# Kernel optimization log

Hardware: AMD Instinct MI355X
Metric: run time of the kernel (lower is better)

## Reference

```python
import jax, jax.numpy as jnp
import numpy as np

N = 512       # num_nodes (feature dim of x == num_nodes, per GCNConv(num_nodes, f1))
BZ = 32       # subjects
TC = 256      # tc_length
F1 = 256
F2 = 128
E = 524288    # edges in the given (corr) graph over all bz*N nodes
NTOT = BZ * N
SLOPE = 0.2   # leaky relu negative_slope


def setup_inputs() -> dict:
    key = jax.random.key(0)
    ks = jax.random.split(key, 17)
    w = lambda k, shape: (jax.random.normal(k, shape, jnp.float32) * (shape[-1] ** -0.5))
    return {
        "x": jax.random.normal(ks[0], (NTOT, N), jnp.float32),
        "t": jax.random.normal(ks[1], (NTOT, TC), jnp.float32),
        "gumbel_u": jax.random.uniform(ks[2], (BZ, N, N, 2), jnp.float32),
        "edge_index": jax.random.randint(ks[3], (2, E), 0, NTOT, jnp.int64 if jax.config.jax_enable_x64 else jnp.int32),
        "conv1_w": w(ks[4], (F1, N)),
        "conv1_b": jnp.zeros((F1,), jnp.float32),
        "conv2_w": w(ks[5], (F2, F1)),
        "conv2_b": jnp.zeros((F2,), jnp.float32),
        "fc_cat_w": w(ks[6], (2, 2 * TC)),
        "fc_cat_b": jnp.zeros((2,), jnp.float32),
        "fcn1_w": w(ks[7], (256, F2 * 2 * N)),
        "fcn1_b": jnp.zeros((256,), jnp.float32),
        "fcn2_w": w(ks[8], (32, 256)),
        "fcn2_b": jnp.zeros((32,), jnp.float32),
        "fcn3_w": w(ks[9], (2, 32)),
        "fcn3_b": jnp.zeros((2,), jnp.float32),
    }


def _gcn_dense(x, A, W, b):
    # PyG GCNConv on a dense 0/1 adjacency A (edge r->c means A[r,c]=1):
    # add self loop, in-degree symmetric norm, aggregate sources into targets.
    n = A.shape[0]
    Ah = A + jnp.eye(n, dtype=A.dtype)
    deg = Ah.sum(axis=0)                                  # in-degree (targets = cols)
    dis = jnp.where(deg > 0, jax.lax.rsqrt(deg), 0.0)
    M = dis[:, None] * Ah * dis[None, :]                  # M[j,i] = d_j^-1/2 A_hat[j,i] d_i^-1/2
    return M.T @ (x @ W.T) + b


def _gcn_sparse(x, row, col, W, b):
    n = x.shape[0]
    loops = jnp.arange(n, dtype=row.dtype)
    r = jnp.concatenate([row, loops])
    c = jnp.concatenate([col, loops])
    deg = jax.ops.segment_sum(jnp.ones_like(c, x.dtype), c, num_segments=n)
    dis = jnp.where(deg > 0, jax.lax.rsqrt(deg), 0.0)
    norm = dis[r] * dis[c]                                # [E+n]
    xw = x @ W.T                                          # [n, out]
    out = jax.ops.segment_sum(xw[r] * norm[:, None], c, num_segments=n)
    return out + b


def reference(x, t, gumbel_u, edge_index, conv1_w, conv1_b, conv2_w, conv2_b,
              fc_cat_w, fc_cat_b, fcn1_w, fcn1_b, fcn2_w, fcn2_b, fcn3_w, fcn3_b):
    bz = t.shape[0] // N
    tb = t.reshape(bz, N, -1)
    xb = x.reshape(bz, N, -1)
    # fc_cat(relu(cat([senders, receivers]))) factors into per-node terms:
    Ws = fc_cat_w[:, :TC]   # multiplies senders half
    Wr = fc_cat_w[:, TC:]   # multiplies receivers half

    def per_sample(ti, xi, ui):
        u = jax.nn.relu(ti)                               # [N, TC]
        ls = u @ Ws.T                                     # [N, 2] sender term
        lr = u @ Wr.T                                     # [N, 2] receiver term
        # pair k = i*N+j has receiver t_i, sender t_j
        logits = lr[:, None, :] + ls[None, :, :] + fc_cat_b   # [N, N, 2]
        g = -jnp.log(-jnp.log(jnp.clip(ui, 1e-9, 1.0 - 1e-9)))  # Gumbel(0,1)
        y = logits + g                                    # tau = 1
        A = (jnp.argmax(y, axis=-1) == 0).astype(xi.dtype)    # hard sample, class 0 => edge
        A = jax.lax.stop_gradient(A)                      # torch.where -> indices blocks grad
        h = jax.nn.relu(_gcn_dense(xi, A, conv1_w, conv1_b))
        return _gcn_dense(h, A, conv2_w, conv2_b)         # [N, F2]

    x_op = jax.vmap(per_sample)(tb, xb, gumbel_u)         # [bz, N, F2]

    row, col = edge_index[0], edge_index[1]
    x_corr = jax.nn.relu(_gcn_sparse(x, row, col, conv1_w, conv1_b))
    x_corr = _gcn_sparse(x_corr, row, col, conv2_w, conv2_b)   # [bz*N, F2]

    emb = jnp.concatenate([x_op.reshape(-1, F2), x_corr], axis=1)  # [bz*N, 2*F2]
    emb = emb.reshape(bz, -1)                             # [bz, 2*F2*N]
    h = jax.nn.leaky_relu(emb @ fcn1_w.T + fcn1_b, SLOPE)
    h = jax.nn.leaky_relu(h @ fcn2_w.T + fcn2_b, SLOPE)
    return h @ fcn3_w.T + fcn3_b                          # [bz, 2]
```

## Files before the change

kernel.cpp:

```cpp
#include <hip/hip_runtime.h>
#include <hip/hip_bf16.h>

typedef __bf16 bf16_t;
typedef __bf16 bf16x8 __attribute__((ext_vector_type(8)));
typedef __bf16 bf16x4 __attribute__((ext_vector_type(4)));
typedef float f32x4 __attribute__((ext_vector_type(4)));

constexpr int kN = 512;
constexpr int kBZ = 32;
constexpr int kTC = 256;
constexpr int kE = 524288;
constexpr int kNTOT = 16384;

__global__ __launch_bounds__(256) void k_cvt3(const float* __restrict__ c1w, const float* __restrict__ c2w,
                                              bf16_t* __restrict__ c1b, bf16_t* __restrict__ c2b,
                                              int* __restrict__ counts, float* __restrict__ degsum) {
    int i = blockIdx.x * 256 + threadIdx.x;
    const int n0 = 32768, n1 = n0 + 8192, n2 = n1 + 4096, n3 = n2 + 4096;
    if (i < n0) {
        float4 v = ((const float4*)c1w)[i];
        bf16x4 o = {(bf16_t)v.x, (bf16_t)v.y, (bf16_t)v.z, (bf16_t)v.w};
        ((bf16x4*)c1b)[i] = o;
    } else if (i < n1) {
        int j = i - n0;
        float4 v = ((const float4*)c2w)[j];
        bf16x4 o = {(bf16_t)v.x, (bf16_t)v.y, (bf16_t)v.z, (bf16_t)v.w};
        ((bf16x4*)c2b)[j] = o;
    } else if (i < n2) {
        ((int4*)counts)[i - n1] = make_int4(0, 0, 0, 0);
    } else if (i < n3) {
        ((float4*)degsum)[i - n2] = make_float4(0.f, 0.f, 0.f, 0.f);
    }
}

__global__ __launch_bounds__(256) void k_lsr(const float* __restrict__ tin, const float* __restrict__ fcw,
                                             const float* __restrict__ fcb, float4* __restrict__ lsr) {
    int row = blockIdx.x * 4 + (threadIdx.x >> 6);
    int lane = threadIdx.x & 63;
    const float* tr = tin + (size_t)row * kTC;
    float s0 = 0, s1 = 0, r0 = 0, r1 = 0;
    for (int k = lane; k < kTC; k += 64) {
        float u = fmaxf(tr[k], 0.f);
        s0 += u * fcw[k];
        s1 += u * fcw[512 + k];
        r0 += u * fcw[256 + k];
        r1 += u * fcw[768 + k];
    }
#pragma unroll
    for (int off = 32; off > 0; off >>= 1) {
        s0 += __shfl_down(s0, off); s1 += __shfl_down(s1, off);
        r0 += __shfl_down(r0, off); r1 += __shfl_down(r1, off);
    }
    if (lane == 0) lsr[row] = make_float4(s0 + fcb[0], s1 + fcb[1], r0, r1);
}

__global__ __launch_bounds__(256) void k_adj(const float* __restrict__ gum, const float4* __restrict__ lsr,
                                             bf16_t* __restrict__ AT, float* __restrict__ degsum) {
    int s = blockIdx.z;
    int a0 = blockIdx.y * 64, b0 = blockIdx.x * 64;
    __shared__ bf16_t tile[64][72];
    int t = threadIdx.x;
    int lb = t & 63, ra = t >> 6;
    int b = b0 + lb;
    float4 pb = lsr[s * kN + b];
#pragma unroll 4
    for (int p = 0; p < 16; p++) {
        int a = a0 + p * 4 + ra;
        float4 qa = lsr[s * kN + a];
        const float* g = gum + ((((size_t)s * kN + a) * kN + b) << 1);
        float u0 = fmaxf(g[0], 1e-9f);
        float u1 = fmaxf(g[1], 1e-9f);
        float g0 = -__logf(-__logf(u0));
        float g1 = -__logf(-__logf(u1));
        float v = ((qa.z + pb.x + g0) >= (qa.w + pb.y + g1)) ? 1.f : 0.f;
        if (a == b) v += 1.f;
        tile[lb][p * 4 + ra] = (bf16_t)v;
    }
    __syncthreads();
    int rj = t >> 3, li = (t & 7) * 8;
#pragma unroll
    for (int p = 0; p < 2; p++) {
        int j = p * 32 + rj;
        bf16x8 v = *(const bf16x8*)&tile[j][li];
        *(bf16x8*)(AT + ((size_t)s * kN + b0 + j) * kN + a0 + li) = v;
        float ps = 0;
#pragma unroll
        for (int q = 0; q < 8; q++) ps += (float)v[q];
        ps += __shfl_down(ps, 4);
        ps += __shfl_down(ps, 2);
        ps += __shfl_down(ps, 1);
        if ((t & 7) == 0) atomicAdd(degsum + s * kN + b0 + j, ps);
    }
}

template <int MODE>
__global__ __launch_bounds__(256) void k_gemm(const bf16_t* __restrict__ A, const bf16_t* __restrict__ B,
                                              bf16_t* __restrict__ C, int K, int lda, int ldb, int ldc,
                                              size_t sA, size_t sB, size_t sC,
                                              const float* __restrict__ degsum, const float* __restrict__ bias) {
    int m0 = blockIdx.x * 128, n0 = blockIdx.y * 128, s = blockIdx.z;
    A += sA * s; B += sB * s; C += sC * s;
    __shared__ bf16_t As[128][72], Bs[128][72];
    f32x4 acc[4][4] = {};
    int tid = threadIdx.x;
    int wave = tid >> 6, lane = tid & 63;
    int wm = (wave & 1) * 64, wn = (wave >> 1) * 64;
    int fm = lane & 15, fq = lane >> 4;
    int srow = tid >> 3, scol = (tid & 7) * 8;
    for (int kb = 0; kb < K; kb += 64) {
        __syncthreads();
#pragma unroll
        for (int p = 0; p < 4; p++) {
            int row = p * 32 + srow;
            *(uint4*)&As[row][scol] = *(const uint4*)(A + (size_t)(m0 + row) * lda + kb + scol);
            *(uint4*)&Bs[row][scol] = *(const uint4*)(B + (size_t)(n0 + row) * ldb + kb + scol);
        }
        __syncthreads();
#pragma unroll
        for (int kk = 0; kk < 2; kk++) {
            bf16x8 af[4], bfr[4];
#pragma unroll
            for (int i = 0; i < 4; i++) {
                af[i] = *(const bf16x8*)&As[wm + i * 16 + fm][kk * 32 + fq * 8];
                bfr[i] = *(const bf16x8*)&Bs[wn + i * 16 + fm][kk * 32 + fq * 8];
            }
#pragma unroll
            for (int i = 0; i < 4; i++)
#pragma unroll
                for (int j = 0; j < 4; j++)
                    acc[i][j] = __builtin_amdgcn_mfma_f32_16x16x32_bf16(af[i], bfr[j], acc[i][j], 0, 0, 0);
        }
    }
#pragma unroll
    for (int i = 0; i < 4; i++) {
#pragma unroll
        for (int r = 0; r < 4; r++) {
            int row = wm + i * 16 + fq * 4 + r;
            float sc = rsqrtf(degsum[(size_t)s * kN + m0 + row]);
#pragma unroll
            for (int j = 0; j < 4; j++) {
                int col = n0 + wn + j * 16 + fm;
                float v = sc * acc[i][j][r] + bias[col];
                if constexpr (MODE == 1) v = fmaxf(v, 0.f);
                C[(size_t)(m0 + row) * ldc + col] = (bf16_t)v;
            }
        }
    }
}

template <bool AF32, int F, int DENSE_ROWS>
__global__ __launch_bounds__(256) void k_gemmT(const void* __restrict__ Ap, const bf16_t* __restrict__ B,
                                               bf16_t* __restrict__ XW, bf16_t* __restrict__ ZT, int K,
                                               const float* __restrict__ degsum) {
    int m0 = blockIdx.x * 128, n0 = blockIdx.y * 128;
    __shared__ __align__(16) bf16_t smem[2 * 128 * 72];
    bf16_t* AsBase = smem;
    bf16_t* BsBase = smem + 128 * 72;
    f32x4 acc[4][4] = {};
    int tid = threadIdx.x;
    int wave = tid >> 6, lane = tid & 63;
    int wm = (wave & 1) * 64, wn = (wave >> 1) * 64;
    int fm = lane & 15, fq = lane >> 4;
    int srow = tid >> 3, scol = (tid & 7) * 8;
    for (int kb = 0; kb < K; kb += 64) {
        __syncthreads();
#pragma unroll
        for (int p = 0; p < 4; p++) {
            int row = p * 32 + srow;
            if constexpr (AF32) {
                const float* ap = (const float*)Ap + (size_t)(m0 + row) * K + kb + scol;
                float4 lo = *(const float4*)ap;
                float4 hi = *(const float4*)(ap + 4);
                bf16x8 o = {(bf16_t)lo.x, (bf16_t)lo.y, (bf16_t)lo.z, (bf16_t)lo.w,
                            (bf16_t)hi.x, (bf16_t)hi.y, (bf16_t)hi.z, (bf16_t)hi.w};
                *(bf16x8*)&AsBase[row * 72 + scol] = o;
            } else {
                *(uint4*)&AsBase[row * 72 + scol] =
                    *(const uint4*)((const bf16_t*)Ap + (size_t)(m0 + row) * K + kb + scol);
            }
            *(uint4*)&BsBase[row * 72 + scol] = *(const uint4*)(B + (size_t)(n0 + row) * K + kb + scol);
        }
        __syncthreads();
#pragma unroll
        for (int kk = 0; kk < 2; kk++) {
            bf16x8 af[4], bfr[4];
#pragma unroll
            for (int i = 0; i < 4; i++) {
                af[i] = *(const bf16x8*)&AsBase[(wm + i * 16 + fm) * 72 + kk * 32 + fq * 8];
                bfr[i] = *(const bf16x8*)&BsBase[(wn + i * 16 + fm) * 72 + kk * 32 + fq * 8];
            }
#pragma unroll
            for (int i = 0; i < 4; i++)
#pragma unroll
                for (int j = 0; j < 4; j++)
                    acc[i][j] = __builtin_amdgcn_mfma_f32_16x16x32_bf16(af[i], bfr[j], acc[i][j], 0, 0, 0);
        }
    }
    bool doT = (m0 < DENSE_ROWS);
    __syncthreads();
#pragma unroll
    for (int i = 0; i < 4; i++) {
#pragma unroll
        for (int r = 0; r < 4; r++) {
            int row = wm + i * 16 + fq * 4 + r;
            float sc = doT ? rsqrtf(degsum[m0 + row]) : 0.f;
#pragma unroll
            for (int j = 0; j < 4; j++) {
                int col = wn + j * 16 + fm;
                float v = acc[i][j][r];
                XW[(size_t)(m0 + row) * F + n0 + col] = (bf16_t)v;
                if (doT) smem[col * 136 + row] = (bf16_t)(sc * v);
            }
        }
    }
    if (doT) {
        __syncthreads();
        int fr = tid >> 1, hi = (tid & 1) * 64;
        bf16_t* zrow = ZT + ((size_t)(m0 >> 9) * F + n0 + fr) * kN + (m0 & 511) + hi;
#pragma unroll
        for (int q = 0; q < 8; q++)
            *(bf16x8*)(zrow + q * 8) = *(const bf16x8*)&smem[fr * 136 + hi + q * 8];
    }
}


__global__ __launch_bounds__(256) void k_hist(const int* __restrict__ col, int* __restrict__ counts) {
    int e = blockIdx.x * 256 + threadIdx.x;
    if (e < kE) atomicAdd(&counts[col[e]], 1);
}

__global__ __launch_bounds__(256) void k_scan(const int* __restrict__ counts, int* __restrict__ offsets,
                                              int* __restrict__ cursor, float* __restrict__ dis_s) {
    __shared__ int ldc_[16896];
    __shared__ int sums[256];
    int t = threadIdx.x;
#define IDX(j) ((j) + ((j) >> 5))
    for (int i = 0; i < 64; i++) {
        int g = i * 256 + t;
        int c = counts[g];
        ldc_[IDX(g)] = c;
        dis_s[g] = rsqrtf((float)(c + 1));
    }
    __syncthreads();
    int s = 0;
    for (int i = 0; i < 64; i++) s += ldc_[IDX(t * 64 + i)];
    sums[t] = s;
    __syncthreads();
    for (int off = 1; off < 256; off <<= 1) {
        int y = (t >= off) ? sums[t - off] : 0;
        __syncthreads();
        sums[t] += y;
        __syncthreads();
    }
    int run = sums[t] - s;
    for (int i = 0; i < 64; i++) {
        int j = t * 64 + i;
        int c = ldc_[IDX(j)];
        ldc_[IDX(j)] = run;
        run += c;
    }
    __syncthreads();
    for (int i = 0; i < 64; i++) {
        int g = i * 256 + t;
        int o = ldc_[IDX(g)];
        offsets[g] = o;
        cursor[g] = o;
    }
#undef IDX
}

__global__ __launch_bounds__(256) void k_fill(const int* __restrict__ row, const int* __restrict__ col,
                                              int* __restrict__ cursor, int* __restrict__ list) {
    int e = blockIdx.x * 256 + threadIdx.x;
    if (e < kE) {
        int p = atomicAdd(&cursor[col[e]], 1);
        list[p] = row[e];
    }
}

template <int F, bool RELU>
__global__ __launch_bounds__(256) void k_sagg(const bf16_t* __restrict__ XW, int rowOffIn,
                                              const int* __restrict__ list, const int* __restrict__ offsets,
                                              const int* __restrict__ counts, const float* __restrict__ dis_s,
                                              const float* __restrict__ bias, bf16_t* __restrict__ OUT,
                                              int outColOff) {
    constexpr int TPR = F / 8;
    constexpr int RPB = 256 / TPR;
    int j = blockIdx.x * RPB + threadIdx.x / TPR;
    int f8 = (threadIdx.x % TPR) * 8;
    float dj = dis_s[j];
    const bf16_t* base = XW + (size_t)rowOffIn * F;
    float acc[8];
    {
        bf16x8 v = *(const bf16x8*)(base + (size_t)j * F + f8);
#pragma unroll
        for (int q = 0; q < 8; q++) acc[q] = dj * (float)v[q];
    }
    int off = offsets[j], cnt = counts[j];
    int e = 0;
    for (; e + 4 <= cnt; e += 4) {
        int r0 = list[off + e], r1 = list[off + e + 1], r2 = list[off + e + 2], r3 = list[off + e + 3];
        float d0 = dis_s[r0], d1 = dis_s[r1], d2 = dis_s[r2], d3 = dis_s[r3];
        bf16x8 v0 = *(const bf16x8*)(base + (size_t)r0 * F + f8);
        bf16x8 v1 = *(const bf16x8*)(base + (size_t)r1 * F + f8);
        bf16x8 v2 = *(const bf16x8*)(base + (size_t)r2 * F + f8);
        bf16x8 v3 = *(const bf16x8*)(base + (size_t)r3 * F + f8);
#pragma unroll
        for (int q = 0; q < 8; q++)
            acc[q] += (d0 * (float)v0[q] + d1 * (float)v1[q]) + (d2 * (float)v2[q] + d3 * (float)v3[q]);
    }
    for (; e < cnt; e++) {
        int r = list[off + e];
        float d = dis_s[r];
        bf16x8 v = *(const bf16x8*)(base + (size_t)r * F + f8);
#pragma unroll
        for (int q = 0; q < 8; q++) acc[q] += d * (float)v[q];
    }
    bf16x8 o;
#pragma unroll
    for (int q = 0; q < 8; q++) {
        float v = dj * acc[q] + bias[f8 + q];
        if (RELU) v = fmaxf(v, 0.f);
        o[q] = (bf16_t)v;
    }
    *(bf16x8*)(OUT + (size_t)j * 256 + outColOff + f8) = o;
}

__global__ __launch_bounds__(256) void k_fcn1(const bf16_t* __restrict__ EMB, const float* __restrict__ W1,
                                              float* __restrict__ partials) {
    int tid = threadIdx.x, wave = tid >> 6, lane = tid & 63;
    int fm = lane & 15, fq = lane >> 4;
    int kb0 = blockIdx.x * 128;
    f32x4 acc[2][4] = {};
#pragma unroll
    for (int ks = 0; ks < 128; ks += 32) {
        int k = kb0 + ks + fq * 8;
        bf16x8 a0 = *(const bf16x8*)(EMB + (size_t)fm * 131072 + k);
        bf16x8 a1 = *(const bf16x8*)(EMB + (size_t)(16 + fm) * 131072 + k);
        bf16x8 bfr[4];
#pragma unroll
        for (int j = 0; j < 4; j++) {
            int n = wave * 64 + j * 16 + fm;
            const float* p = W1 + (size_t)n * 131072 + k;
            float4 lo = *(const float4*)p;
            float4 hi = *(const float4*)(p + 4);
            bf16x8 b = {(bf16_t)lo.x, (bf16_t)lo.y, (bf16_t)lo.z, (bf16_t)lo.w,
                        (bf16_t)hi.x, (bf16_t)hi.y, (bf16_t)hi.z, (bf16_t)hi.w};
            bfr[j] = b;
        }
#pragma unroll
        for (int j = 0; j < 4; j++) {
            acc[0][j] = __builtin_amdgcn_mfma_f32_16x16x32_bf16(a0, bfr[j], acc[0][j], 0, 0, 0);
            acc[1][j] = __builtin_amdgcn_mfma_f32_16x16x32_bf16(a1, bfr[j], acc[1][j], 0, 0, 0);
        }
    }
    float* P = partials + (size_t)blockIdx.x * 8192;
#pragma unroll
    for (int i = 0; i < 2; i++)
#pragma unroll
        for (int j = 0; j < 4; j++)
#pragma unroll
            for (int r = 0; r < 4; r++)
                P[(size_t)(i * 16 + fq * 4 + r) * 256 + wave * 64 + j * 16 + fm] = acc[i][j][r];
}

__global__ __launch_bounds__(256) void k_reduce(const float* __restrict__ partials, float* __restrict__ part2) {
    int kg = blockIdx.x >> 5, eb = blockIdx.x & 31;
    int e = eb * 256 + threadIdx.x;
    float s = 0;
#pragma unroll 8
    for (int i = 0; i < 128; i++) s += partials[(size_t)(kg * 128 + i) * 8192 + e];
    part2[(size_t)kg * 8192 + e] = s;
}

__global__ __launch_bounds__(256) void k_head(const float* __restrict__ part2, const float* __restrict__ b1,
                                              const float* __restrict__ W2, const float* __restrict__ b2,
                                              const float* __restrict__ W3, const float* __restrict__ b3,
                                              float* __restrict__ out) {
    __shared__ float h1s[32][256];
    __shared__ float h2s[32][32];
    int t = threadIdx.x;
    for (int i = 0; i < 32; i++) {
        int e = i * 256 + t;
        float s = 0;
#pragma unroll
        for (int kg = 0; kg < 8; kg++) s += part2[kg * 8192 + e];
        s += b1[t];
        h1s[i][t] = (s > 0.f) ? s : 0.2f * s;
    }
    __syncthreads();
    for (int p = 0; p < 4; p++) {
        int id = p * 256 + t, si = id >> 5, o2 = id & 31;
        float s = 0;
        for (int k = 0; k < 256; k++) s += h1s[si][k] * W2[o2 * 256 + k];
        s += b2[o2];
        h2s[si][o2] = (s > 0.f) ? s : 0.2f * s;
    }
    __syncthreads();
    if (t < 64) {
        int si = t >> 1, o3 = t & 1;
        float s = 0;
#pragma unroll
        for (int k = 0; k < 32; k++) s += h2s[si][k] * W3[o3 * 32 + k];
        out[si * 2 + o3] = s + b3[o3];
    }
}


extern "C" void kernel_launch(void* const* d_in, const int* in_sizes, int n_in,
                              void* d_out, int out_size, void* d_ws, size_t ws_size,
                              hipStream_t stream) {
    const float* x = (const float*)d_in[0];
    const float* t = (const float*)d_in[1];
    const float* gum = (const float*)d_in[2];
    const int* eidx = (const int*)d_in[3];
    const float* c1w = (const float*)d_in[4];
    const float* c1b = (const float*)d_in[5];
    const float* c2w = (const float*)d_in[6];
    const float* c2b = (const float*)d_in[7];
    const float* fcw = (const float*)d_in[8];
    const float* fcb = (const float*)d_in[9];
    const float* w1 = (const float*)d_in[10];
    const float* b1 = (const float*)d_in[11];
    const float* w2 = (const float*)d_in[12];
    const float* b2 = (const float*)d_in[13];
    const float* w3 = (const float*)d_in[14];
    const float* b3 = (const float*)d_in[15];
    float* out = (float*)d_out;
    (void)in_sizes; (void)n_in; (void)out_size; (void)ws_size;

    char* ws = (char*)d_ws;
    size_t off = 0;
    auto alloc = [&](size_t bytes) -> char* {
        char* p = ws + off;
        off += (bytes + 255) & ~size_t(255);
        return p;
    };
    bf16_t* c1wb = (bf16_t*)alloc((size_t)256 * 512 * 2);
    bf16_t* c2wb = (bf16_t*)alloc((size_t)128 * 256 * 2);
    float4* lsr = (float4*)alloc((size_t)kNTOT * 16);
    bf16_t* AT = (bf16_t*)alloc((size_t)kBZ * kN * kN * 2);
    float* degsum = (float*)alloc((size_t)kNTOT * 4);
    bf16_t* XW1_EMB = (bf16_t*)alloc((size_t)kNTOT * 256 * 2);
    bf16_t* Z1T = (bf16_t*)alloc((size_t)kBZ * 256 * 512 * 2);
    bf16_t* H = (bf16_t*)alloc((size_t)32768 * 256 * 2);
    bf16_t* XW2 = (bf16_t*)alloc((size_t)32768 * 128 * 2);
    bf16_t* Z2T = (bf16_t*)alloc((size_t)kBZ * 128 * 512 * 2);
    int* counts = (int*)alloc((size_t)kNTOT * 4);
    int* offsets = (int*)alloc((size_t)kNTOT * 4);
    int* cursor = (int*)alloc((size_t)kNTOT * 4);
    float* diss = (float*)alloc((size_t)kNTOT * 4);
    int* list = (int*)alloc((size_t)kE * 4);
    float* partials = (float*)alloc((size_t)1024 * 8192 * 4);
    float* part2 = (float*)alloc((size_t)8 * 8192 * 4);

    bf16_t* XW1 = XW1_EMB;
    bf16_t* EMB = XW1_EMB;

    k_cvt3<<<192, 256, 0, stream>>>(c1w, c2w, c1wb, c2wb, counts, degsum);
    k_lsr<<<4096, 256, 0, stream>>>(t, fcw, fcb, lsr);
    k_adj<<<dim3(8, 8, 32), 256, 0, stream>>>(gum, lsr, AT, degsum);
    k_hist<<<2048, 256, 0, stream>>>(eidx + kE, counts);
    k_scan<<<1, 256, 0, stream>>>(counts, offsets, cursor, diss);
    k_fill<<<2048, 256, 0, stream>>>(eidx, eidx + kE, cursor, list);
    k_gemmT<true, 256, kNTOT><<<dim3(128, 2, 1), 256, 0, stream>>>(x, c1wb, XW1, Z1T, 512, degsum);
    k_gemm<1><<<dim3(4, 2, 32), 256, 0, stream>>>(AT, Z1T, H, 512, 512, 512, 256,
                                                  (size_t)512 * 512, (size_t)256 * 512, (size_t)512 * 256,
                                                  degsum, c1b);
    k_sagg<256, true><<<2048, 256, 0, stream>>>(XW1, 0, list, offsets, counts, diss, c1b,
                                                H + (size_t)16384 * 256, 0);
    k_gemmT<false, 128, kNTOT><<<dim3(256, 1, 1), 256, 0, stream>>>(H, c2wb, XW2, Z2T, 256, degsum);
    k_gemm<2><<<dim3(4, 1, 32), 256, 0, stream>>>(AT, Z2T, EMB, 512, 512, 512, 256,
                                                  (size_t)512 * 512, (size_t)128 * 512, (size_t)512 * 256,
                                                  degsum, c2b);
    k_sagg<128, false><<<1024, 256, 0, stream>>>(XW2, 16384, list, offsets, counts, diss, c2b, EMB, 128);
    k_fcn1<<<1024, 256, 0, stream>>>(EMB, w1, partials);
    k_reduce<<<256, 256, 0, stream>>>(partials, part2);
    k_head<<<1, 256, 0, stream>>>(part2, b1, w2, b2, w3, b3, out);
}
```

Before: 517.3 us.

## Merge dense and sparse GCN aggregation launches and pre-convert fcn1 weights in spare blocks

Merges the prep kernels (lsr and weight conversion) into a single launch. Each GCN layer's batched dense adjacency GEMM and its sparse edge-gather aggregation now run as block ranges of one kernel, so the two independent paths share a launch and fill the GPU together. The layer-1 launch also carries extra blocks that convert the large fcn1 weight (fp32) to bf16 into a new buffer, and fcn1 then reads bf16 instead of converting on the fly. This halves fcn1's weight traffic. In exchange it adds a full fp32 read and bf16 write of that weight, plus mixes heterogeneous block types in one kernel.

```diff
diff --git a/kernel.cpp b/kernel.cpp
--- a/kernel.cpp
+++ b/kernel.cpp
@@ -12,46 +12,48 @@
 constexpr int kE = 524288;
 constexpr int kNTOT = 16384;
 
-__global__ __launch_bounds__(256) void k_cvt3(const float* __restrict__ c1w, const float* __restrict__ c2w,
-                                              bf16_t* __restrict__ c1b, bf16_t* __restrict__ c2b,
+__global__ __launch_bounds__(256) void k_prep(const float* __restrict__ tin, const float* __restrict__ fcw,
+                                              const float* __restrict__ fcb, float4* __restrict__ lsr,
+                                              const float* __restrict__ c1w, const float* __restrict__ c2w,
+                                              bf16_t* __restrict__ c1wb, bf16_t* __restrict__ c2wb,
                                               int* __restrict__ counts, float* __restrict__ degsum) {
-    int i = blockIdx.x * 256 + threadIdx.x;
-    const int n0 = 32768, n1 = n0 + 8192, n2 = n1 + 4096, n3 = n2 + 4096;
-    if (i < n0) {
-        float4 v = ((const float4*)c1w)[i];
-        bf16x4 o = {(bf16_t)v.x, (bf16_t)v.y, (bf16_t)v.z, (bf16_t)v.w};
-        ((bf16x4*)c1b)[i] = o;
-    } else if (i < n1) {
-        int j = i - n0;
-        float4 v = ((const float4*)c2w)[j];
-        bf16x4 o = {(bf16_t)v.x, (bf16_t)v.y, (bf16_t)v.z, (bf16_t)v.w};
-        ((bf16x4*)c2b)[j] = o;
-    } else if (i < n2) {
-        ((int4*)counts)[i - n1] = make_int4(0, 0, 0, 0);
-    } else if (i < n3) {
-        ((float4*)degsum)[i - n2] = make_float4(0.f, 0.f, 0.f, 0.f);
-    }
-}
-
-__global__ __launch_bounds__(256) void k_lsr(const float* __restrict__ tin, const float* __restrict__ fcw,
-                                             const float* __restrict__ fcb, float4* __restrict__ lsr) {
-    int row = blockIdx.x * 4 + (threadIdx.x >> 6);
-    int lane = threadIdx.x & 63;
-    const float* tr = tin + (size_t)row * kTC;
-    float s0 = 0, s1 = 0, r0 = 0, r1 = 0;
-    for (int k = lane; k < kTC; k += 64) {
-        float u = fmaxf(tr[k], 0.f);
-        s0 += u * fcw[k];
-        s1 += u * fcw[512 + k];
-        r0 += u * fcw[256 + k];
-        r1 += u * fcw[768 + k];
-    }
-#pragma unroll
-    for (int off = 32; off > 0; off >>= 1) {
-        s0 += __shfl_down(s0, off); s1 += __shfl_down(s1, off);
-        r0 += __shfl_down(r0, off); r1 += __shfl_down(r1, off);
-    }
-    if (lane == 0) lsr[row] = make_float4(s0 + fcb[0], s1 + fcb[1], r0, r1);
+    int b = blockIdx.x;
+    if (b < 4096) {
+        int row = b * 4 + (threadIdx.x >> 6);
+        int lane = threadIdx.x & 63;
+        const float* tr = tin + (size_t)row * kTC;
+        float s0 = 0, s1 = 0, r0 = 0, r1 = 0;
+        for (int k = lane; k < kTC; k += 64) {
+            float u = fmaxf(tr[k], 0.f);
+            s0 += u * fcw[k];
+            s1 += u * fcw[512 + k];
+            r0 += u * fcw[256 + k];
+            r1 += u * fcw[768 + k];
+        }
+#pragma unroll
+        for (int off = 32; off > 0; off >>= 1) {
+            s0 += __shfl_down(s0, off); s1 += __shfl_down(s1, off);
+            r0 += __shfl_down(r0, off); r1 += __shfl_down(r1, off);
+        }
+        if (lane == 0) lsr[row] = make_float4(s0 + fcb[0], s1 + fcb[1], r0, r1);
+    } else {
+        int i = (b - 4096) * 256 + threadIdx.x;
+        const int n0 = 32768, n1 = n0 + 8192, n2 = n1 + 4096, n3 = n2 + 4096;
+        if (i < n0) {
+            float4 v = ((const float4*)c1w)[i];
+            bf16x4 o = {(bf16_t)v.x, (bf16_t)v.y, (bf16_t)v.z, (bf16_t)v.w};
+            ((bf16x4*)c1wb)[i] = o;
+        } else if (i < n1) {
+            int j = i - n0;
+            float4 v = ((const float4*)c2w)[j];
+            bf16x4 o = {(bf16_t)v.x, (bf16_t)v.y, (bf16_t)v.z, (bf16_t)v.w};
+            ((bf16x4*)c2wb)[j] = o;
+        } else if (i < n2) {
+            ((int4*)counts)[i - n1] = make_int4(0, 0, 0, 0);
+        } else if (i < n3) {
+            ((float4*)degsum)[i - n2] = make_float4(0.f, 0.f, 0.f, 0.f);
+        }
+    }
 }
 
 __global__ __launch_bounds__(256) void k_adj(const float* __restrict__ gum, const float4* __restrict__ lsr,
@@ -93,61 +95,6 @@
     }
 }
 
-template <int MODE>
-__global__ __launch_bounds__(256) void k_gemm(const bf16_t* __restrict__ A, const bf16_t* __restrict__ B,
-                                              bf16_t* __restrict__ C, int K, int lda, int ldb, int ldc,
-                                              size_t sA, size_t sB, size_t sC,
-                                              const float* __restrict__ degsum, const float* __restrict__ bias) {
-    int m0 = blockIdx.x * 128, n0 = blockIdx.y * 128, s = blockIdx.z;
-    A += sA * s; B += sB * s; C += sC * s;
-    __shared__ bf16_t As[128][72], Bs[128][72];
-    f32x4 acc[4][4] = {};
-    int tid = threadIdx.x;
-    int wave = tid >> 6, lane = tid & 63;
-    int wm = (wave & 1) * 64, wn = (wave >> 1) * 64;
-    int fm = lane & 15, fq = lane >> 4;
-    int srow = tid >> 3, scol = (tid & 7) * 8;
-    for (int kb = 0; kb < K; kb += 64) {
-        __syncthreads();
-#pragma unroll
-        for (int p = 0; p < 4; p++) {
-            int row = p * 32 + srow;
-            *(uint4*)&As[row][scol] = *(const uint4*)(A + (size_t)(m0 + row) * lda + kb + scol);
-            *(uint4*)&Bs[row][scol] = *(const uint4*)(B + (size_t)(n0 + row) * ldb + kb + scol);
-        }
-        __syncthreads();
-#pragma unroll
-        for (int kk = 0; kk < 2; kk++) {
-            bf16x8 af[4], bfr[4];
-#pragma unroll
-            for (int i = 0; i < 4; i++) {
-                af[i] = *(const bf16x8*)&As[wm + i * 16 + fm][kk * 32 + fq * 8];
-                bfr[i] = *(const bf16x8*)&Bs[wn + i * 16 + fm][kk * 32 + fq * 8];
-            }
-#pragma unroll
-            for (int i = 0; i < 4; i++)
-#pragma unroll
-                for (int j = 0; j < 4; j++)
-                    acc[i][j] = __builtin_amdgcn_mfma_f32_16x16x32_bf16(af[i], bfr[j], acc[i][j], 0, 0, 0);
-        }
-    }
-#pragma unroll
-    for (int i = 0; i < 4; i++) {
-#pragma unroll
-        for (int r = 0; r < 4; r++) {
-            int row = wm + i * 16 + fq * 4 + r;
-            float sc = rsqrtf(degsum[(size_t)s * kN + m0 + row]);
-#pragma unroll
-            for (int j = 0; j < 4; j++) {
-                int col = n0 + wn + j * 16 + fm;
-                float v = sc * acc[i][j][r] + bias[col];
-                if constexpr (MODE == 1) v = fmaxf(v, 0.f);
-                C[(size_t)(m0 + row) * ldc + col] = (bf16_t)v;
-            }
-        }
-    }
-}
-
 template <bool AF32, int F, int DENSE_ROWS>
 __global__ __launch_bounds__(256) void k_gemmT(const void* __restrict__ Ap, const bf16_t* __restrict__ B,
                                                bf16_t* __restrict__ XW, bf16_t* __restrict__ ZT, int K,
@@ -278,55 +225,124 @@
     }
 }
 
-template <int F, bool RELU>
-__global__ __launch_bounds__(256) void k_sagg(const bf16_t* __restrict__ XW, int rowOffIn,
-                                              const int* __restrict__ list, const int* __restrict__ offsets,
-                                              const int* __restrict__ counts, const float* __restrict__ dis_s,
-                                              const float* __restrict__ bias, bf16_t* __restrict__ OUT,
-                                              int outColOff) {
-    constexpr int TPR = F / 8;
-    constexpr int RPB = 256 / TPR;
-    int j = blockIdx.x * RPB + threadIdx.x / TPR;
-    int f8 = (threadIdx.x % TPR) * 8;
-    float dj = dis_s[j];
-    const bf16_t* base = XW + (size_t)rowOffIn * F;
-    float acc[8];
-    {
-        bf16x8 v = *(const bf16x8*)(base + (size_t)j * F + f8);
-#pragma unroll
-        for (int q = 0; q < 8; q++) acc[q] = dj * (float)v[q];
-    }
-    int off = offsets[j], cnt = counts[j];
-    int e = 0;
-    for (; e + 4 <= cnt; e += 4) {
-        int r0 = list[off + e], r1 = list[off + e + 1], r2 = list[off + e + 2], r3 = list[off + e + 3];
-        float d0 = dis_s[r0], d1 = dis_s[r1], d2 = dis_s[r2], d3 = dis_s[r3];
-        bf16x8 v0 = *(const bf16x8*)(base + (size_t)r0 * F + f8);
-        bf16x8 v1 = *(const bf16x8*)(base + (size_t)r1 * F + f8);
-        bf16x8 v2 = *(const bf16x8*)(base + (size_t)r2 * F + f8);
-        bf16x8 v3 = *(const bf16x8*)(base + (size_t)r3 * F + f8);
-#pragma unroll
-        for (int q = 0; q < 8; q++)
-            acc[q] += (d0 * (float)v0[q] + d1 * (float)v1[q]) + (d2 * (float)v2[q] + d3 * (float)v3[q]);
-    }
-    for (; e < cnt; e++) {
-        int r = list[off + e];
-        float d = dis_s[r];
-        bf16x8 v = *(const bf16x8*)(base + (size_t)r * F + f8);
-#pragma unroll
-        for (int q = 0; q < 8; q++) acc[q] += d * (float)v[q];
-    }
-    bf16x8 o;
-#pragma unroll
-    for (int q = 0; q < 8; q++) {
-        float v = dj * acc[q] + bias[f8 + q];
-        if (RELU) v = fmaxf(v, 0.f);
-        o[q] = (bf16_t)v;
-    }
-    *(bf16x8*)(OUT + (size_t)j * 256 + outColOff + f8) = o;
-}
-
-__global__ __launch_bounds__(256) void k_fcn1(const bf16_t* __restrict__ EMB, const float* __restrict__ W1,
+template <int GB, int NT, int F, bool RELU, bool CVT>
+__global__ __launch_bounds__(256) void k_layer(const bf16_t* __restrict__ AT, const bf16_t* __restrict__ ZT,
+                                               const float* __restrict__ degsum, const float* __restrict__ bias,
+                                               const bf16_t* __restrict__ gbase, const int* __restrict__ list,
+                                               const int* __restrict__ offsets, const int* __restrict__ counts,
+                                               const float* __restrict__ dis_s, const float* __restrict__ w1,
+                                               bf16_t* __restrict__ w1b, bf16_t* __restrict__ OUT, int outColOff) {
+    __shared__ __align__(16) bf16_t smem[2 * 128 * 72];
+    int b = blockIdx.x;
+    int tid = threadIdx.x;
+    constexpr int NGATHER = (kNTOT * (F / 8)) / 256;
+    if (b < GB) {
+        int m0 = (b & 3) * 128, n0 = ((b >> 2) & (NT - 1)) * 128, s = b >> (NT == 2 ? 3 : 2);
+        const bf16_t* A = AT + (size_t)s * 512 * 512;
+        const bf16_t* B = ZT + (size_t)s * F * 512;
+        bf16_t* C = OUT + (size_t)s * 512 * 256;
+        bf16_t* As = smem;
+        bf16_t* Bs = smem + 128 * 72;
+        f32x4 acc[4][4] = {};
+        int wave = tid >> 6, lane = tid & 63;
+        int wm = (wave & 1) * 64, wn = (wave >> 1) * 64;
+        int fm = lane & 15, fq = lane >> 4;
+        int srow = tid >> 3, scol = (tid & 7) * 8;
+        for (int kb = 0; kb < 512; kb += 64) {
+            __syncthreads();
+#pragma unroll
+            for (int p = 0; p < 4; p++) {
+                int row = p * 32 + srow;
+                *(uint4*)&As[row * 72 + scol] = *(const uint4*)(A + (size_t)(m0 + row) * 512 + kb + scol);
+                *(uint4*)&Bs[row * 72 + scol] = *(const uint4*)(B + (size_t)(n0 + row) * 512 + kb + scol);
+            }
+            __syncthreads();
+#pragma unroll
+            for (int kk = 0; kk < 2; kk++) {
+                bf16x8 af[4], bfr[4];
+#pragma unroll
+                for (int i = 0; i < 4; i++) {
+                    af[i] = *(const bf16x8*)&As[(wm + i * 16 + fm) * 72 + kk * 32 + fq * 8];
+                    bfr[i] = *(const bf16x8*)&Bs[(wn + i * 16 + fm) * 72 + kk * 32 + fq * 8];
+                }
+#pragma unroll
+                for (int i = 0; i < 4; i++)
+#pragma unroll
+                    for (int j = 0; j < 4; j++)
+                        acc[i][j] = __builtin_amdgcn_mfma_f32_16x16x32_bf16(af[i], bfr[j], acc[i][j], 0, 0, 0);
+            }
+        }
+#pragma unroll
+        for (int i = 0; i < 4; i++) {
+#pragma unroll
+            for (int r = 0; r < 4; r++) {
+                int row = wm + i * 16 + fq * 4 + r;
+                float sc = rsqrtf(degsum[(size_t)s * kN + m0 + row]);
+#pragma unroll
+                for (int j = 0; j < 4; j++) {
+                    int col = n0 + wn + j * 16 + fm;
+                    float v = sc * acc[i][j][r] + bias[col];
+                    if (RELU) v = fmaxf(v, 0.f);
+                    C[(size_t)(m0 + row) * 256 + col] = (bf16_t)v;
+                }
+            }
+        }
+    } else if (b < GB + NGATHER) {
+        constexpr int TPR = F / 8;
+        constexpr int RPB = 256 / TPR;
+        int j = (b - GB) * RPB + tid / TPR;
+        int f8 = (tid % TPR) * 8;
+        float dj = dis_s[j];
+        float acc[8];
+        {
+            bf16x8 v = *(const bf16x8*)(gbase + (size_t)j * F + f8);
+#pragma unroll
+            for (int q = 0; q < 8; q++) acc[q] = dj * (float)v[q];
+        }
+        int off = offsets[j], cnt = counts[j];
+        int e = 0;
+        for (; e + 4 <= cnt; e += 4) {
+            int r0 = list[off + e], r1 = list[off + e + 1], r2 = list[off + e + 2], r3 = list[off + e + 3];
+            float d0 = dis_s[r0], d1 = dis_s[r1], d2 = dis_s[r2], d3 = dis_s[r3];
+            bf16x8 v0 = *(const bf16x8*)(gbase + (size_t)r0 * F + f8);
+            bf16x8 v1 = *(const bf16x8*)(gbase + (size_t)r1 * F + f8);
+            bf16x8 v2 = *(const bf16x8*)(gbase + (size_t)r2 * F + f8);
+            bf16x8 v3 = *(const bf16x8*)(gbase + (size_t)r3 * F + f8);
+#pragma unroll
+            for (int q = 0; q < 8; q++)
+                acc[q] += (d0 * (float)v0[q] + d1 * (float)v1[q]) + (d2 * (float)v2[q] + d3 * (float)v3[q]);
+        }
+        for (; e < cnt; e++) {
+            int r = list[off + e];
+            float d = dis_s[r];
+            bf16x8 v = *(const bf16x8*)(gbase + (size_t)r * F + f8);
+#pragma unroll
+            for (int q = 0; q < 8; q++) acc[q] += d * (float)v[q];
+        }
+        bf16x8 o;
+#pragma unroll
+        for (int q = 0; q < 8; q++) {
+            float v = dj * acc[q] + bias[f8 + q];
+            if (RELU) v = fmaxf(v, 0.f);
+            o[q] = (bf16_t)v;
+        }
+        bf16_t* orow = RELU ? (OUT + (size_t)(16384 + j) * 256) : (OUT + (size_t)j * 256);
+        *(bf16x8*)(orow + outColOff + f8) = o;
+    } else if (CVT) {
+        int base = (b - GB - NGATHER) * 8192 + tid;
+        const float4* src = (const float4*)w1;
+        bf16x4* dst = (bf16x4*)w1b;
+#pragma unroll 4
+        for (int i = 0; i < 32; i++) {
+            int idx = base + i * 256;
+            float4 v = src[idx];
+            bf16x4 o = {(bf16_t)v.x, (bf16_t)v.y, (bf16_t)v.z, (bf16_t)v.w};
+            dst[idx] = o;
+        }
+    }
+}
+
+__global__ __launch_bounds__(256) void k_fcn1(const bf16_t* __restrict__ EMB, const bf16_t* __restrict__ W1B,
                                               float* __restrict__ partials) {
     int tid = threadIdx.x, wave = tid >> 6, lane = tid & 63;
     int fm = lane & 15, fq = lane >> 4;
@@ -341,12 +357,7 @@
 #pragma unroll
         for (int j = 0; j < 4; j++) {
             int n = wave * 64 + j * 16 + fm;
-            const float* p = W1 + (size_t)n * 131072 + k;
-            float4 lo = *(const float4*)p;
-            float4 hi = *(const float4*)(p + 4);
-            bf16x8 b = {(bf16_t)lo.x, (bf16_t)lo.y, (bf16_t)lo.z, (bf16_t)lo.w,
-                        (bf16_t)hi.x, (bf16_t)hi.y, (bf16_t)hi.z, (bf16_t)hi.w};
-            bfr[j] = b;
+            bfr[j] = *(const bf16x8*)(W1B + (size_t)n * 131072 + k);
         }
 #pragma unroll
         for (int j = 0; j < 4; j++) {
@@ -446,6 +457,7 @@
     bf16_t* H = (bf16_t*)alloc((size_t)32768 * 256 * 2);
     bf16_t* XW2 = (bf16_t*)alloc((size_t)32768 * 128 * 2);
     bf16_t* Z2T = (bf16_t*)alloc((size_t)kBZ * 128 * 512 * 2);
+    bf16_t* w1b = (bf16_t*)alloc((size_t)256 * 131072 * 2);
     int* counts = (int*)alloc((size_t)kNTOT * 4);
     int* offsets = (int*)alloc((size_t)kNTOT * 4);
     int* cursor = (int*)alloc((size_t)kNTOT * 4);
@@ -457,24 +469,19 @@
     bf16_t* XW1 = XW1_EMB;
     bf16_t* EMB = XW1_EMB;
 
-    k_cvt3<<<192, 256, 0, stream>>>(c1w, c2w, c1wb, c2wb, counts, degsum);
-    k_lsr<<<4096, 256, 0, stream>>>(t, fcw, fcb, lsr);
+    k_prep<<<4288, 256, 0, stream>>>(t, fcw, fcb, lsr, c1w, c2w, c1wb, c2wb, counts, degsum);
     k_adj<<<dim3(8, 8, 32), 256, 0, stream>>>(gum, lsr, AT, degsum);
     k_hist<<<2048, 256, 0, stream>>>(eidx + kE, counts);
     k_scan<<<1, 256, 0, stream>>>(counts, offsets, cursor, diss);
     k_fill<<<2048, 256, 0, stream>>>(eidx, eidx + kE, cursor, list);
     k_gemmT<true, 256, kNTOT><<<dim3(128, 2, 1), 256, 0, stream>>>(x, c1wb, XW1, Z1T, 512, degsum);
-    k_gemm<1><<<dim3(4, 2, 32), 256, 0, stream>>>(AT, Z1T, H, 512, 512, 512, 256,
-                                                  (size_t)512 * 512, (size_t)256 * 512, (size_t)512 * 256,
-                                                  degsum, c1b);
-    k_sagg<256, true><<<2048, 256, 0, stream>>>(XW1, 0, list, offsets, counts, diss, c1b,
-                                                H + (size_t)16384 * 256, 0);
+    k_layer<256, 2, 256, true, true><<<3328, 256, 0, stream>>>(AT, Z1T, degsum, c1b, XW1, list, offsets,
+                                                               counts, diss, w1, w1b, H, 0);
     k_gemmT<false, 128, kNTOT><<<dim3(256, 1, 1), 256, 0, stream>>>(H, c2wb, XW2, Z2T, 256, degsum);
-    k_gemm<2><<<dim3(4, 1, 32), 256, 0, stream>>>(AT, Z2T, EMB, 512, 512, 512, 256,
-                                                  (size_t)512 * 512, (size_t)128 * 512, (size_t)512 * 256,
-                                                  degsum, c2b);
-    k_sagg<128, false><<<1024, 256, 0, stream>>>(XW2, 16384, list, offsets, counts, diss, c2b, EMB, 128);
-    k_fcn1<<<1024, 256, 0, stream>>>(EMB, w1, partials);
+    k_layer<128, 1, 128, false, false><<<1152, 256, 0, stream>>>(AT, Z2T, degsum, c2b,
+                                                                 XW2 + (size_t)16384 * 128, list, offsets,
+                                                                 counts, diss, nullptr, nullptr, EMB, 128);
+    k_fcn1<<<1024, 256, 0, stream>>>(EMB, w1b, partials);
     k_reduce<<<256, 256, 0, stream>>>(partials, part2);
     k_head<<<1, 256, 0, stream>>>(part2, b1, w2, b2, w3, b3, out);
 }
```

Result: slower. 546.3 us (+5.6%).
